# Performance work log

Hardware: AMD Instinct MI355X
Metric: run time of the kernel (lower is better)

The kernel has to match this reference:

```python
import jax, jax.numpy as jnp
import numpy as np


def setup_inputs() -> dict:
    key = jax.random.key(0)
    k1, k2, k3, k4 = jax.random.split(key, 4)
    B, Q, K, H, D = 2, 2048, 2048, 16, 128
    qs = jax.random.normal(k1, (B, Q, H, D), dtype=jnp.float32)
    ks = jax.random.normal(k2, (B, K, H, D), dtype=jnp.float32)
    vs = jax.random.normal(k3, (B, K, H, D), dtype=jnp.float32)
    valid_lens = jax.random.randint(k4, (B,), 1, K + 1, dtype=jnp.int32)
    return {"qs": qs, "ks": ks, "vs": vs, "valid_lens": valid_lens}


def reference(qs, ks, vs, valid_lens):
    B, Q, H, D = qs.shape
    K = ks.shape[1]
    # rearrange 'B L H D -> (B H) L D'
    q = qs.transpose(0, 2, 1, 3).reshape(B * H, Q, D)
    k = ks.transpose(0, 2, 1, 3).reshape(B * H, K, D)
    v = vs.transpose(0, 2, 1, 3).reshape(B * H, K, D)
    # DotScorer: scaled dot product -> (B*H, Q, K)
    scores = jnp.einsum('bqd,bkd->bqk', q, k) / jnp.sqrt(jnp.float32(D))
    # mask_attn: key positions >= valid_len get large negative score
    vl = jnp.repeat(valid_lens, H)                         # (B*H,)
    mask = jnp.arange(K)[None, None, :] < vl[:, None, None]
    scores = jnp.where(mask, scores, jnp.float32(-1e6))
    attn = jax.nn.softmax(scores, axis=-1)
    # dropout is identity (p_dropout=0 / not training)
    ctx = attn @ v                                         # (B*H, Q, D)
    ctx = ctx.reshape(B, H, Q, D).transpose(0, 2, 1, 3)    # (B, Q, H, D)
    return ctx, attn.reshape(B, H, Q, K)
```

## Files before the change

kernel.cpp:

```cpp
#include <hip/hip_runtime.h>
#include <hip/hip_bf16.h>
#include <stdint.h>

#define B_ 2
#define Qn 2048
#define Kn 2048
#define Hn 16
#define Dn 128
#define QT 128
#define KT 64
#define KT1 128
#define HD (Hn*Dn)
#define KROW 132
#define VROW 72

typedef __bf16 bf16x8 __attribute__((ext_vector_type(8)));
typedef __bf16 bf16x4 __attribute__((ext_vector_type(4)));
typedef float f32x4 __attribute__((ext_vector_type(4)));

union BF8 { __bf16 e[8]; bf16x8 v; };

#define SCALE 0.088388347648318447f

struct SMp2 { unsigned short K[2][KT][KROW]; unsigned short V[2][Dn][VROW]; };
union SMu { SMp2 p2; unsigned short K1[2][KT1][KROW]; };

__device__ __forceinline__ void bar_lgkm() {
  asm volatile("s_waitcnt lgkmcnt(0)" ::: "memory");
  __builtin_amdgcn_s_barrier();
  __builtin_amdgcn_sched_barrier(0);
}

__device__ __forceinline__ bf16x4 cvt4(f32x4 a) {
  bf16x4 r;
  r[0] = (__bf16)a[0]; r[1] = (__bf16)a[1];
  r[2] = (__bf16)a[2]; r[3] = (__bf16)a[3];
  return r;
}

__device__ __forceinline__ void stage_k64(const float* kb, unsigned short (*dst)[KROW], int tid) {
  #pragma unroll
  for (int ii = 0; ii < 4; ++ii) {
    int chunk = ii * 512 + tid;
    int row = chunk >> 5, cv = chunk & 31;
    f32x4 a = *(const f32x4*)(kb + (size_t)row * HD + cv * 4);
    *(bf16x4*)&dst[row][cv * 4] = cvt4(a);
  }
}

__device__ __forceinline__ void stage_k128(const float* kb, unsigned short (*dst)[KROW], int tid) {
  #pragma unroll
  for (int ii = 0; ii < 8; ++ii) {
    int chunk = ii * 512 + tid;
    int row = chunk >> 5, cv = chunk & 31;
    f32x4 a = *(const f32x4*)(kb + (size_t)row * HD + cv * 4);
    *(bf16x4*)&dst[row][cv * 4] = cvt4(a);
  }
}

__device__ __forceinline__ void stage_v64(const float* vb, unsigned short (*dst)[VROW], int tid) {
  int d = tid & 127, t0 = tid >> 7;
  const float* colp = vb + d;
  #pragma unroll
  for (int rr = 0; rr < 2; ++rr) {
    int idx = rr * 4 + t0;
    int kk = idx >> 2, gg = idx & 3;
    int kb0 = kk * 32 + gg * 4;
    BF8 t;
    #pragma unroll
    for (int j = 0; j < 4; ++j) {
      t.e[j]     = (__bf16)colp[(size_t)(kb0 + j) * HD];
      t.e[4 + j] = (__bf16)colp[(size_t)(kb0 + 16 + j) * HD];
    }
    *(bf16x8*)&dst[d][kk * 32 + gg * 8] = t.v;
  }
}

__device__ __forceinline__ void load_q(const float* qrow, BF8* qf, int g) {
  #pragma unroll
  for (int s = 0; s < 4; ++s) {
    f32x4 a0 = *(const f32x4*)(qrow + s * 32 + g * 8);
    f32x4 a1 = *(const f32x4*)(qrow + s * 32 + g * 8 + 4);
    #pragma unroll
    for (int j = 0; j < 4; ++j) { qf[s].e[j] = (__bf16)a0[j]; qf[s].e[4 + j] = (__bf16)a1[j]; }
  }
}

__global__ __launch_bounds__(512, 4) void attn_fwd(
    const float* __restrict__ qs, const float* __restrict__ ks,
    const float* __restrict__ vs, const int* __restrict__ vlen,
    float* __restrict__ ctx_out, float* __restrict__ attn_out)
{
  __shared__ __align__(16) SMu sm;

  const int tid = threadIdx.x, wave = tid >> 6, lane = tid & 63;
  const int c = lane & 15, g = lane >> 4;

  const int L   = blockIdx.x;
  const int xcd = L & 7;
  const int i5  = L >> 3;
  const int bh  = ((i5 & 3) << 3) + xcd;
  const int qt  = i5 >> 2;
  const int b   = bh >> 4, h = bh & 15;
  const int vl  = vlen[b];
  const int qb  = qt * QT + wave * 16;

  BF8 qf[4];
  load_q(qs + (((size_t)(b * Qn + qb + c)) * Hn + h) * Dn, qf, g);
  const float* kbase = ks + ((size_t)b * Kn * Hn + h) * Dn;
  const float* vbase = vs + ((size_t)b * Kn * Hn + h) * Dn;

  float rs = 0.f;
  {
    const int nkt = (vl + KT1 - 1) / KT1;
    stage_k128(kbase, sm.K1[0], tid);
    bar_lgkm();
    for (int t = 0; t < nkt; ++t) {
      const int cur = t & 1;
      if (t + 1 < nkt) stage_k128(kbase + (size_t)(t + 1) * KT1 * HD, sm.K1[cur ^ 1], tid);
      #pragma unroll
      for (int nt = 0; nt < 8; ++nt) {
        f32x4 acc = {0.f, 0.f, 0.f, 0.f};
        #pragma unroll
        for (int s = 0; s < 4; ++s) {
          BF8 kf; kf.v = *(const bf16x8*)&sm.K1[cur][nt * 16 + c][s * 32 + g * 8];
          acc = __builtin_amdgcn_mfma_f32_16x16x32_bf16(kf.v, qf[s].v, acc, 0, 0, 0);
        }
        const int k0 = t * KT1 + nt * 16 + g * 4;
        #pragma unroll
        for (int r = 0; r < 4; ++r)
          rs += (k0 + r < vl) ? __expf(acc[r] * SCALE) : 0.f;
      }
      bar_lgkm();
    }
  }
  rs += __shfl_xor(rs, 16);
  rs += __shfl_xor(rs, 32);
  const float inv = 1.0f / rs;

  f32x4 ctxa[8];
  #pragma unroll
  for (int ii = 0; ii < 8; ++ii) ctxa[ii] = (f32x4){0.f, 0.f, 0.f, 0.f};

  const int nkt = (vl + KT - 1) / KT;
  stage_k64(kbase, sm.p2.K[0], tid);
  stage_v64(vbase, sm.p2.V[0], tid);
  bar_lgkm();
  float* rowp = attn_out + ((size_t)bh * Qn + qb + c) * Kn;
  for (int t = 0; t < nkt; ++t) {
    const int cur = t & 1;
    if (t + 1 < nkt) {
      stage_k64(kbase + (size_t)(t + 1) * KT * HD, sm.p2.K[cur ^ 1], tid);
      stage_v64(vbase + (size_t)(t + 1) * KT * HD, sm.p2.V[cur ^ 1], tid);
    }
    BF8 pf[2];
    #pragma unroll
    for (int nt = 0; nt < 4; ++nt) {
      f32x4 acc = {0.f, 0.f, 0.f, 0.f};
      #pragma unroll
      for (int s = 0; s < 4; ++s) {
        BF8 kf; kf.v = *(const bf16x8*)&sm.p2.K[cur][nt * 16 + c][s * 32 + g * 8];
        acc = __builtin_amdgcn_mfma_f32_16x16x32_bf16(kf.v, qf[s].v, acc, 0, 0, 0);
      }
      const int k0 = t * KT + nt * 16 + g * 4;
      f32x4 p;
      #pragma unroll
      for (int r = 0; r < 4; ++r) {
        p[r] = (k0 + r < vl) ? __expf(acc[r] * SCALE) * inv : 0.f;
        pf[nt >> 1].e[(nt & 1) * 4 + r] = (__bf16)p[r];
      }
      *(f32x4*)(rowp + t * KT + nt * 16 + g * 4) = p;
    }
    #pragma unroll
    for (int kk = 0; kk < 2; ++kk)
      #pragma unroll
      for (int n8 = 0; n8 < 8; ++n8) {
        BF8 vf; vf.v = *(const bf16x8*)&sm.p2.V[cur][n8 * 16 + c][kk * 32 + g * 8];
        ctxa[n8] = __builtin_amdgcn_mfma_f32_16x16x32_bf16(vf.v, pf[kk].v, ctxa[n8], 0, 0, 0);
      }
    bar_lgkm();
  }

  const int col0 = nkt * KT;
  #pragma unroll 1
  for (int r = 0; r < 16; ++r) {
    float* zp = attn_out + ((size_t)bh * Qn + qb + r) * Kn;
    for (int c4 = col0 + lane * 4; c4 < Kn; c4 += 256)
      *(f32x4*)(zp + c4) = (f32x4){0.f, 0.f, 0.f, 0.f};
  }

  float* cp = ctx_out + (((size_t)(b * Qn + qb + c)) * Hn + h) * Dn;
  #pragma unroll
  for (int n8 = 0; n8 < 8; ++n8)
    *(f32x4*)(cp + n8 * 16 + g * 4) = ctxa[n8];
}

extern "C" void kernel_launch(void* const* d_in, const int* in_sizes, int n_in,
                              void* d_out, int out_size, void* d_ws, size_t ws_size,
                              hipStream_t stream) {
  const float* qs   = (const float*)d_in[0];
  const float* ks   = (const float*)d_in[1];
  const float* vs   = (const float*)d_in[2];
  const int*   vlen = (const int*)d_in[3];
  float* ctx  = (float*)d_out;
  float* attn = ctx + (size_t)B_ * Qn * Hn * Dn;
  attn_fwd<<<dim3((Qn / QT) * B_ * Hn), 512, 0, stream>>>(qs, ks, vs, vlen, ctx, attn);
}
```

Measured before the change: 217.3 us.

## Switch attention kernel to 32x32x16 MFMA with 256-query and 128-key tiles

Moves both the row-sum pass and the output pass from 16x16x32 to 32x32x16 bf16 MFMA. Each wave now handles 32 query rows, the block covers 256 queries, and both passes use 128-key tiles with matching K/V shared layouts. The aim is more reuse of each staged K/V tile across queries and fewer LDS reads per MFMA, so K/V staging traffic and grid size drop. The cost is more registers and LDS per block, with occupancy lowered to 2 blocks per CU, and only 256 blocks in the grid.

```diff
diff --git a/kernel.cpp b/kernel.cpp
--- a/kernel.cpp
+++ b/kernel.cpp
@@ -7,23 +7,25 @@
 #define Kn 2048
 #define Hn 16
 #define Dn 128
-#define QT 128
-#define KT 64
-#define KT1 128
+#define QT 256
+#define KT 128
 #define HD (Hn*Dn)
 #define KROW 132
-#define VROW 72
+#define VROW 136
 
 typedef __bf16 bf16x8 __attribute__((ext_vector_type(8)));
 typedef __bf16 bf16x4 __attribute__((ext_vector_type(4)));
 typedef float f32x4 __attribute__((ext_vector_type(4)));
+typedef float f32x16 __attribute__((ext_vector_type(16)));
 
 union BF8 { __bf16 e[8]; bf16x8 v; };
 
 #define SCALE 0.088388347648318447f
 
-struct SMp2 { unsigned short K[2][KT][KROW]; unsigned short V[2][Dn][VROW]; };
-union SMu { SMp2 p2; unsigned short K1[2][KT1][KROW]; };
+struct SMs {
+  unsigned short K[2][KT][KROW];
+  unsigned short V[2][Dn][VROW];
+};
 
 __device__ __forceinline__ void bar_lgkm() {
   asm volatile("s_waitcnt lgkmcnt(0)" ::: "memory");
@@ -38,17 +40,7 @@
   return r;
 }
 
-__device__ __forceinline__ void stage_k64(const float* kb, unsigned short (*dst)[KROW], int tid) {
-  #pragma unroll
-  for (int ii = 0; ii < 4; ++ii) {
-    int chunk = ii * 512 + tid;
-    int row = chunk >> 5, cv = chunk & 31;
-    f32x4 a = *(const f32x4*)(kb + (size_t)row * HD + cv * 4);
-    *(bf16x4*)&dst[row][cv * 4] = cvt4(a);
-  }
-}
-
-__device__ __forceinline__ void stage_k128(const float* kb, unsigned short (*dst)[KROW], int tid) {
+__device__ __forceinline__ void stage_k(const float* kb, unsigned short (*dst)[KROW], int tid) {
   #pragma unroll
   for (int ii = 0; ii < 8; ++ii) {
     int chunk = ii * 512 + tid;
@@ -58,43 +50,32 @@
   }
 }
 
-__device__ __forceinline__ void stage_v64(const float* vb, unsigned short (*dst)[VROW], int tid) {
-  int d = tid & 127, t0 = tid >> 7;
+__device__ __forceinline__ void stage_v(const float* vb, unsigned short (*dst)[VROW], int tid) {
+  int d = tid & 127, c0 = tid >> 7;
   const float* colp = vb + d;
   #pragma unroll
-  for (int rr = 0; rr < 2; ++rr) {
-    int idx = rr * 4 + t0;
-    int kk = idx >> 2, gg = idx & 3;
-    int kb0 = kk * 32 + gg * 4;
+  for (int rr = 0; rr < 4; ++rr) {
+    int idx = rr * 4 + c0;
+    int base = (idx >> 2) * 32 + ((idx >> 1) & 1) * 16 + (idx & 1) * 4;
     BF8 t;
     #pragma unroll
     for (int j = 0; j < 4; ++j) {
-      t.e[j]     = (__bf16)colp[(size_t)(kb0 + j) * HD];
-      t.e[4 + j] = (__bf16)colp[(size_t)(kb0 + 16 + j) * HD];
-    }
-    *(bf16x8*)&dst[d][kk * 32 + gg * 8] = t.v;
-  }
-}
-
-__device__ __forceinline__ void load_q(const float* qrow, BF8* qf, int g) {
-  #pragma unroll
-  for (int s = 0; s < 4; ++s) {
-    f32x4 a0 = *(const f32x4*)(qrow + s * 32 + g * 8);
-    f32x4 a1 = *(const f32x4*)(qrow + s * 32 + g * 8 + 4);
-    #pragma unroll
-    for (int j = 0; j < 4; ++j) { qf[s].e[j] = (__bf16)a0[j]; qf[s].e[4 + j] = (__bf16)a1[j]; }
-  }
-}
-
-__global__ __launch_bounds__(512, 4) void attn_fwd(
+      t.e[j]     = (__bf16)colp[(size_t)(base + j) * HD];
+      t.e[4 + j] = (__bf16)colp[(size_t)(base + 8 + j) * HD];
+    }
+    *(bf16x8*)&dst[d][idx * 8] = t.v;
+  }
+}
+
+__global__ __launch_bounds__(512, 2) void attn_fwd(
     const float* __restrict__ qs, const float* __restrict__ ks,
     const float* __restrict__ vs, const int* __restrict__ vlen,
     float* __restrict__ ctx_out, float* __restrict__ attn_out)
 {
-  __shared__ __align__(16) SMu sm;
+  __shared__ __align__(16) SMs sm;
 
   const int tid = threadIdx.x, wave = tid >> 6, lane = tid & 63;
-  const int c = lane & 15, g = lane >> 4;
+  const int l31 = lane & 31, hi = lane >> 5;
 
   const int L   = blockIdx.x;
   const int xcd = L & 7;
@@ -103,96 +84,123 @@
   const int qt  = i5 >> 2;
   const int b   = bh >> 4, h = bh & 15;
   const int vl  = vlen[b];
-  const int qb  = qt * QT + wave * 16;
-
-  BF8 qf[4];
-  load_q(qs + (((size_t)(b * Qn + qb + c)) * Hn + h) * Dn, qf, g);
+  const int qbw = qt * QT + wave * 32;
+
+  BF8 qf[8];
+  {
+    const float* qrow = qs + (((size_t)(b * Qn + qbw + l31)) * Hn + h) * Dn;
+    #pragma unroll
+    for (int s = 0; s < 8; ++s) {
+      int d0 = s * 16 + hi * 8;
+      f32x4 a0 = *(const f32x4*)(qrow + d0);
+      f32x4 a1 = *(const f32x4*)(qrow + d0 + 4);
+      #pragma unroll
+      for (int j = 0; j < 4; ++j) { qf[s].e[j] = (__bf16)a0[j]; qf[s].e[4 + j] = (__bf16)a1[j]; }
+    }
+  }
+
   const float* kbase = ks + ((size_t)b * Kn * Hn + h) * Dn;
   const float* vbase = vs + ((size_t)b * Kn * Hn + h) * Dn;
+  const int nkt = (vl + KT - 1) / KT;
 
   float rs = 0.f;
-  {
-    const int nkt = (vl + KT1 - 1) / KT1;
-    stage_k128(kbase, sm.K1[0], tid);
+  stage_k(kbase, sm.K[0], tid);
+  bar_lgkm();
+  for (int t = 0; t < nkt; ++t) {
+    const int cur = t & 1;
+    if (t + 1 < nkt) stage_k(kbase + (size_t)(t + 1) * KT * HD, sm.K[cur ^ 1], tid);
+    #pragma unroll
+    for (int m = 0; m < 4; ++m) {
+      f32x16 acc;
+      #pragma unroll
+      for (int i = 0; i < 16; ++i) acc[i] = 0.f;
+      #pragma unroll
+      for (int s = 0; s < 8; ++s) {
+        BF8 kf; kf.v = *(const bf16x8*)&sm.K[cur][m * 32 + l31][s * 16 + hi * 8];
+        acc = __builtin_amdgcn_mfma_f32_32x32x16_bf16(kf.v, qf[s].v, acc, 0, 0, 0);
+      }
+      const int kb0 = t * KT + m * 32 + hi * 4;
+      #pragma unroll
+      for (int reg = 0; reg < 16; ++reg) {
+        int key = kb0 + (reg & 3) + 8 * (reg >> 2);
+        rs += (key < vl) ? __expf(acc[reg] * SCALE) : 0.f;
+      }
+    }
     bar_lgkm();
-    for (int t = 0; t < nkt; ++t) {
-      const int cur = t & 1;
-      if (t + 1 < nkt) stage_k128(kbase + (size_t)(t + 1) * KT1 * HD, sm.K1[cur ^ 1], tid);
-      #pragma unroll
-      for (int nt = 0; nt < 8; ++nt) {
-        f32x4 acc = {0.f, 0.f, 0.f, 0.f};
-        #pragma unroll
-        for (int s = 0; s < 4; ++s) {
-          BF8 kf; kf.v = *(const bf16x8*)&sm.K1[cur][nt * 16 + c][s * 32 + g * 8];
-          acc = __builtin_amdgcn_mfma_f32_16x16x32_bf16(kf.v, qf[s].v, acc, 0, 0, 0);
-        }
-        const int k0 = t * KT1 + nt * 16 + g * 4;
-        #pragma unroll
-        for (int r = 0; r < 4; ++r)
-          rs += (k0 + r < vl) ? __expf(acc[r] * SCALE) : 0.f;
-      }
-      bar_lgkm();
-    }
-  }
-  rs += __shfl_xor(rs, 16);
+  }
   rs += __shfl_xor(rs, 32);
   const float inv = 1.0f / rs;
 
-  f32x4 ctxa[8];
-  #pragma unroll
-  for (int ii = 0; ii < 8; ++ii) ctxa[ii] = (f32x4){0.f, 0.f, 0.f, 0.f};
-
-  const int nkt = (vl + KT - 1) / KT;
-  stage_k64(kbase, sm.p2.K[0], tid);
-  stage_v64(vbase, sm.p2.V[0], tid);
+  f32x16 ctxa[4];
+  #pragma unroll
+  for (int ch = 0; ch < 4; ++ch)
+    #pragma unroll
+    for (int i = 0; i < 16; ++i) ctxa[ch][i] = 0.f;
+
+  stage_k(kbase, sm.K[0], tid);
+  stage_v(vbase, sm.V[0], tid);
   bar_lgkm();
-  float* rowp = attn_out + ((size_t)bh * Qn + qb + c) * Kn;
+  float* rowp = attn_out + ((size_t)bh * Qn + qbw + l31) * Kn;
   for (int t = 0; t < nkt; ++t) {
     const int cur = t & 1;
     if (t + 1 < nkt) {
-      stage_k64(kbase + (size_t)(t + 1) * KT * HD, sm.p2.K[cur ^ 1], tid);
-      stage_v64(vbase + (size_t)(t + 1) * KT * HD, sm.p2.V[cur ^ 1], tid);
-    }
-    BF8 pf[2];
-    #pragma unroll
-    for (int nt = 0; nt < 4; ++nt) {
-      f32x4 acc = {0.f, 0.f, 0.f, 0.f};
-      #pragma unroll
-      for (int s = 0; s < 4; ++s) {
-        BF8 kf; kf.v = *(const bf16x8*)&sm.p2.K[cur][nt * 16 + c][s * 32 + g * 8];
-        acc = __builtin_amdgcn_mfma_f32_16x16x32_bf16(kf.v, qf[s].v, acc, 0, 0, 0);
-      }
-      const int k0 = t * KT + nt * 16 + g * 4;
-      f32x4 p;
-      #pragma unroll
-      for (int r = 0; r < 4; ++r) {
-        p[r] = (k0 + r < vl) ? __expf(acc[r] * SCALE) * inv : 0.f;
-        pf[nt >> 1].e[(nt & 1) * 4 + r] = (__bf16)p[r];
-      }
-      *(f32x4*)(rowp + t * KT + nt * 16 + g * 4) = p;
-    }
-    #pragma unroll
-    for (int kk = 0; kk < 2; ++kk)
-      #pragma unroll
-      for (int n8 = 0; n8 < 8; ++n8) {
-        BF8 vf; vf.v = *(const bf16x8*)&sm.p2.V[cur][n8 * 16 + c][kk * 32 + g * 8];
-        ctxa[n8] = __builtin_amdgcn_mfma_f32_16x16x32_bf16(vf.v, pf[kk].v, ctxa[n8], 0, 0, 0);
-      }
+      stage_k(kbase + (size_t)(t + 1) * KT * HD, sm.K[cur ^ 1], tid);
+      stage_v(vbase + (size_t)(t + 1) * KT * HD, sm.V[cur ^ 1], tid);
+    }
+    #pragma unroll
+    for (int m = 0; m < 4; ++m) {
+      f32x16 acc;
+      #pragma unroll
+      for (int i = 0; i < 16; ++i) acc[i] = 0.f;
+      #pragma unroll
+      for (int s = 0; s < 8; ++s) {
+        BF8 kf; kf.v = *(const bf16x8*)&sm.K[cur][m * 32 + l31][s * 16 + hi * 8];
+        acc = __builtin_amdgcn_mfma_f32_32x32x16_bf16(kf.v, qf[s].v, acc, 0, 0, 0);
+      }
+      const int kb0 = t * KT + m * 32;
+      BF8 pf0, pf1;
+      #pragma unroll
+      for (int r4 = 0; r4 < 4; ++r4) {
+        f32x4 p;
+        #pragma unroll
+        for (int rr = 0; rr < 4; ++rr) {
+          int key = kb0 + r4 * 8 + hi * 4 + rr;
+          float v = (key < vl) ? __expf(acc[r4 * 4 + rr] * SCALE) * inv : 0.f;
+          p[rr] = v;
+          if (r4 < 2) pf0.e[r4 * 4 + rr] = (__bf16)v;
+          else        pf1.e[(r4 - 2) * 4 + rr] = (__bf16)v;
+        }
+        *(f32x4*)(rowp + kb0 + r4 * 8 + hi * 4) = p;
+      }
+      #pragma unroll
+      for (int ch = 0; ch < 4; ++ch) {
+        BF8 v0; v0.v = *(const bf16x8*)&sm.V[cur][ch * 32 + l31][(m * 4 + hi) * 8];
+        ctxa[ch] = __builtin_amdgcn_mfma_f32_32x32x16_bf16(v0.v, pf0.v, ctxa[ch], 0, 0, 0);
+        BF8 v1; v1.v = *(const bf16x8*)&sm.V[cur][ch * 32 + l31][(m * 4 + 2 + hi) * 8];
+        ctxa[ch] = __builtin_amdgcn_mfma_f32_32x32x16_bf16(v1.v, pf1.v, ctxa[ch], 0, 0, 0);
+      }
+    }
     bar_lgkm();
   }
 
   const int col0 = nkt * KT;
   #pragma unroll 1
-  for (int r = 0; r < 16; ++r) {
-    float* zp = attn_out + ((size_t)bh * Qn + qb + r) * Kn;
+  for (int r = 0; r < 32; ++r) {
+    float* zp = attn_out + ((size_t)bh * Qn + qbw + r) * Kn;
     for (int c4 = col0 + lane * 4; c4 < Kn; c4 += 256)
       *(f32x4*)(zp + c4) = (f32x4){0.f, 0.f, 0.f, 0.f};
   }
 
-  float* cp = ctx_out + (((size_t)(b * Qn + qb + c)) * Hn + h) * Dn;
-  #pragma unroll
-  for (int n8 = 0; n8 < 8; ++n8)
-    *(f32x4*)(cp + n8 * 16 + g * 4) = ctxa[n8];
+  float* cp = ctx_out + (((size_t)(b * Qn + qbw + l31)) * Hn + h) * Dn;
+  #pragma unroll
+  for (int ch = 0; ch < 4; ++ch)
+    #pragma unroll
+    for (int r4 = 0; r4 < 4; ++r4) {
+      f32x4 o;
+      #pragma unroll
+      for (int rr = 0; rr < 4; ++rr) o[rr] = ctxa[ch][r4 * 4 + rr];
+      *(f32x4*)(cp + ch * 32 + r4 * 8 + hi * 4) = o;
+    }
 }
 
 extern "C" void kernel_launch(void* const* d_in, const int* in_sizes, int n_in,
```

Result: no change. 215.6 us (-0.8%).

## Split K/V staging into register prefetch and deferred LDS write

Applied to the files above, without the earlier changes.

Global loads of the next K/V tile now go into registers before the compute of the current tile. The bf16 conversion and LDS store happen only after the MFMA work, so load latency overlaps with compute instead of stalling at the staging point. It also raises wave priority with s_setprio around the compute section. The cost is higher register pressure, with 32 floats for K128 and 32 for K64+V, which could spill or reduce occupancy under launch_bounds(512,4).

```diff
diff --git a/kernel.cpp b/kernel.cpp
--- a/kernel.cpp
+++ b/kernel.cpp
@@ -38,40 +38,62 @@
   return r;
 }
 
-__device__ __forceinline__ void stage_k64(const float* kb, unsigned short (*dst)[KROW], int tid) {
+__device__ __forceinline__ void load_k64_raw(const float* kb, int tid, f32x4* r) {
   #pragma unroll
   for (int ii = 0; ii < 4; ++ii) {
     int chunk = ii * 512 + tid;
     int row = chunk >> 5, cv = chunk & 31;
-    f32x4 a = *(const f32x4*)(kb + (size_t)row * HD + cv * 4);
-    *(bf16x4*)&dst[row][cv * 4] = cvt4(a);
-  }
-}
-
-__device__ __forceinline__ void stage_k128(const float* kb, unsigned short (*dst)[KROW], int tid) {
+    r[ii] = *(const f32x4*)(kb + (size_t)row * HD + cv * 4);
+  }
+}
+__device__ __forceinline__ void write_k64(const f32x4* r, unsigned short (*dst)[KROW], int tid) {
+  #pragma unroll
+  for (int ii = 0; ii < 4; ++ii) {
+    int chunk = ii * 512 + tid;
+    int row = chunk >> 5, cv = chunk & 31;
+    *(bf16x4*)&dst[row][cv * 4] = cvt4(r[ii]);
+  }
+}
+
+__device__ __forceinline__ void load_k128_raw(const float* kb, int tid, f32x4* r) {
   #pragma unroll
   for (int ii = 0; ii < 8; ++ii) {
     int chunk = ii * 512 + tid;
     int row = chunk >> 5, cv = chunk & 31;
-    f32x4 a = *(const f32x4*)(kb + (size_t)row * HD + cv * 4);
-    *(bf16x4*)&dst[row][cv * 4] = cvt4(a);
-  }
-}
-
-__device__ __forceinline__ void stage_v64(const float* vb, unsigned short (*dst)[VROW], int tid) {
+    r[ii] = *(const f32x4*)(kb + (size_t)row * HD + cv * 4);
+  }
+}
+__device__ __forceinline__ void write_k128(const f32x4* r, unsigned short (*dst)[KROW], int tid) {
+  #pragma unroll
+  for (int ii = 0; ii < 8; ++ii) {
+    int chunk = ii * 512 + tid;
+    int row = chunk >> 5, cv = chunk & 31;
+    *(bf16x4*)&dst[row][cv * 4] = cvt4(r[ii]);
+  }
+}
+
+__device__ __forceinline__ void load_v64_raw(const float* vb, int tid, float* r) {
+  int t0 = tid >> 7;
+  const float* colp = vb + (tid & 127);
+  #pragma unroll
+  for (int rr = 0; rr < 2; ++rr) {
+    int idx = rr * 4 + t0, kk = idx >> 2, gg = idx & 3;
+    int kb0 = kk * 32 + gg * 4;
+    #pragma unroll
+    for (int j = 0; j < 4; ++j) {
+      r[rr * 8 + j]     = colp[(size_t)(kb0 + j) * HD];
+      r[rr * 8 + 4 + j] = colp[(size_t)(kb0 + 16 + j) * HD];
+    }
+  }
+}
+__device__ __forceinline__ void write_v64(const float* r, unsigned short (*dst)[VROW], int tid) {
   int d = tid & 127, t0 = tid >> 7;
-  const float* colp = vb + d;
   #pragma unroll
   for (int rr = 0; rr < 2; ++rr) {
-    int idx = rr * 4 + t0;
-    int kk = idx >> 2, gg = idx & 3;
-    int kb0 = kk * 32 + gg * 4;
+    int idx = rr * 4 + t0, kk = idx >> 2, gg = idx & 3;
     BF8 t;
     #pragma unroll
-    for (int j = 0; j < 4; ++j) {
-      t.e[j]     = (__bf16)colp[(size_t)(kb0 + j) * HD];
-      t.e[4 + j] = (__bf16)colp[(size_t)(kb0 + 16 + j) * HD];
-    }
+    for (int j = 0; j < 8; ++j) t.e[j] = (__bf16)r[rr * 8 + j];
     *(bf16x8*)&dst[d][kk * 32 + gg * 8] = t.v;
   }
 }
@@ -113,11 +135,15 @@
   float rs = 0.f;
   {
     const int nkt = (vl + KT1 - 1) / KT1;
-    stage_k128(kbase, sm.K1[0], tid);
+    f32x4 kr[8];
+    load_k128_raw(kbase, tid, kr);
+    write_k128(kr, sm.K1[0], tid);
     bar_lgkm();
     for (int t = 0; t < nkt; ++t) {
       const int cur = t & 1;
-      if (t + 1 < nkt) stage_k128(kbase + (size_t)(t + 1) * KT1 * HD, sm.K1[cur ^ 1], tid);
+      const bool pf = (t + 1 < nkt);
+      if (pf) load_k128_raw(kbase + (size_t)(t + 1) * KT1 * HD, tid, kr);
+      __builtin_amdgcn_s_setprio(1);
       #pragma unroll
       for (int nt = 0; nt < 8; ++nt) {
         f32x4 acc = {0.f, 0.f, 0.f, 0.f};
@@ -131,6 +157,8 @@
         for (int r = 0; r < 4; ++r)
           rs += (k0 + r < vl) ? __expf(acc[r] * SCALE) : 0.f;
       }
+      __builtin_amdgcn_s_setprio(0);
+      if (pf) write_k128(kr, sm.K1[cur ^ 1], tid);
       bar_lgkm();
     }
   }
@@ -143,42 +171,55 @@
   for (int ii = 0; ii < 8; ++ii) ctxa[ii] = (f32x4){0.f, 0.f, 0.f, 0.f};
 
   const int nkt = (vl + KT - 1) / KT;
-  stage_k64(kbase, sm.p2.K[0], tid);
-  stage_v64(vbase, sm.p2.V[0], tid);
-  bar_lgkm();
-  float* rowp = attn_out + ((size_t)bh * Qn + qb + c) * Kn;
-  for (int t = 0; t < nkt; ++t) {
-    const int cur = t & 1;
-    if (t + 1 < nkt) {
-      stage_k64(kbase + (size_t)(t + 1) * KT * HD, sm.p2.K[cur ^ 1], tid);
-      stage_v64(vbase + (size_t)(t + 1) * KT * HD, sm.p2.V[cur ^ 1], tid);
+  {
+    f32x4 kr[4];
+    float vr[16];
+    load_k64_raw(kbase, tid, kr);
+    load_v64_raw(vbase, tid, vr);
+    write_k64(kr, sm.p2.K[0], tid);
+    write_v64(vr, sm.p2.V[0], tid);
+    bar_lgkm();
+    float* rowp = attn_out + ((size_t)bh * Qn + qb + c) * Kn;
+    for (int t = 0; t < nkt; ++t) {
+      const int cur = t & 1;
+      const bool pf = (t + 1 < nkt);
+      if (pf) {
+        load_k64_raw(kbase + (size_t)(t + 1) * KT * HD, tid, kr);
+        load_v64_raw(vbase + (size_t)(t + 1) * KT * HD, tid, vr);
+      }
+      __builtin_amdgcn_s_setprio(1);
+      BF8 pfm[2];
+      #pragma unroll
+      for (int nt = 0; nt < 4; ++nt) {
+        f32x4 acc = {0.f, 0.f, 0.f, 0.f};
+        #pragma unroll
+        for (int s = 0; s < 4; ++s) {
+          BF8 kf; kf.v = *(const bf16x8*)&sm.p2.K[cur][nt * 16 + c][s * 32 + g * 8];
+          acc = __builtin_amdgcn_mfma_f32_16x16x32_bf16(kf.v, qf[s].v, acc, 0, 0, 0);
+        }
+        const int k0 = t * KT + nt * 16 + g * 4;
+        f32x4 p;
+        #pragma unroll
+        for (int r = 0; r < 4; ++r) {
+          p[r] = (k0 + r < vl) ? __expf(acc[r] * SCALE) * inv : 0.f;
+          pfm[nt >> 1].e[(nt & 1) * 4 + r] = (__bf16)p[r];
+        }
+        *(f32x4*)(rowp + t * KT + nt * 16 + g * 4) = p;
+      }
+      #pragma unroll
+      for (int kk = 0; kk < 2; ++kk)
+        #pragma unroll
+        for (int n8 = 0; n8 < 8; ++n8) {
+          BF8 vf; vf.v = *(const bf16x8*)&sm.p2.V[cur][n8 * 16 + c][kk * 32 + g * 8];
+          ctxa[n8] = __builtin_amdgcn_mfma_f32_16x16x32_bf16(vf.v, pfm[kk].v, ctxa[n8], 0, 0, 0);
+        }
+      __builtin_amdgcn_s_setprio(0);
+      if (pf) {
+        write_k64(kr, sm.p2.K[cur ^ 1], tid);
+        write_v64(vr, sm.p2.V[cur ^ 1], tid);
+      }
+      bar_lgkm();
     }
-    BF8 pf[2];
-    #pragma unroll
-    for (int nt = 0; nt < 4; ++nt) {
-      f32x4 acc = {0.f, 0.f, 0.f, 0.f};
-      #pragma unroll
-      for (int s = 0; s < 4; ++s) {
-        BF8 kf; kf.v = *(const bf16x8*)&sm.p2.K[cur][nt * 16 + c][s * 32 + g * 8];
-        acc = __builtin_amdgcn_mfma_f32_16x16x32_bf16(kf.v, qf[s].v, acc, 0, 0, 0);
-      }
-      const int k0 = t * KT + nt * 16 + g * 4;
-      f32x4 p;
-      #pragma unroll
-      for (int r = 0; r < 4; ++r) {
-        p[r] = (k0 + r < vl) ? __expf(acc[r] * SCALE) * inv : 0.f;
-        pf[nt >> 1].e[(nt & 1) * 4 + r] = (__bf16)p[r];
-      }
-      *(f32x4*)(rowp + t * KT + nt * 16 + g * 4) = p;
-    }
-    #pragma unroll
-    for (int kk = 0; kk < 2; ++kk)
-      #pragma unroll
-      for (int n8 = 0; n8 < 8; ++n8) {
-        BF8 vf; vf.v = *(const bf16x8*)&sm.p2.V[cur][n8 * 16 + c][kk * 32 + g * 8];
-        ctxa[n8] = __builtin_amdgcn_mfma_f32_16x16x32_bf16(vf.v, pf[kk].v, ctxa[n8], 0, 0, 0);
-      }
-    bar_lgkm();
   }
 
   const int col0 = nkt * KT;
```

New measurement: 223.7 us. 1.03x slower.

## Skew PV matmul one tile behind QK and skip masking on full tiles

Applied to the files above, without the earlier changes.

The second pass now stages V for the current tile while running the P·V MFMAs for the previous tile. This software-pipelines the V transpose-load latency behind the QK and exp work. Both passes also skip the per-element valid-length comparison on every tile except the partial last one. The row-sum uses a 4-wide vector accumulator to shorten the dependency chain. The cost is extra registers for the carried P fragments and a post-loop epilogue, which could hurt occupancy.

```diff
diff --git a/kernel.cpp b/kernel.cpp
--- a/kernel.cpp
+++ b/kernel.cpp
@@ -110,14 +110,16 @@
   const float* kbase = ks + ((size_t)b * Kn * Hn + h) * Dn;
   const float* vbase = vs + ((size_t)b * Kn * Hn + h) * Dn;
 
-  float rs = 0.f;
+  f32x4 rsv = {0.f, 0.f, 0.f, 0.f};
   {
     const int nkt = (vl + KT1 - 1) / KT1;
+    const bool hasb = (vl & (KT1 - 1)) != 0;
     stage_k128(kbase, sm.K1[0], tid);
     bar_lgkm();
     for (int t = 0; t < nkt; ++t) {
       const int cur = t & 1;
       if (t + 1 < nkt) stage_k128(kbase + (size_t)(t + 1) * KT1 * HD, sm.K1[cur ^ 1], tid);
+      const bool mb = hasb && (t == nkt - 1);
       #pragma unroll
       for (int nt = 0; nt < 8; ++nt) {
         f32x4 acc = {0.f, 0.f, 0.f, 0.f};
@@ -126,14 +128,20 @@
           BF8 kf; kf.v = *(const bf16x8*)&sm.K1[cur][nt * 16 + c][s * 32 + g * 8];
           acc = __builtin_amdgcn_mfma_f32_16x16x32_bf16(kf.v, qf[s].v, acc, 0, 0, 0);
         }
-        const int k0 = t * KT1 + nt * 16 + g * 4;
-        #pragma unroll
-        for (int r = 0; r < 4; ++r)
-          rs += (k0 + r < vl) ? __expf(acc[r] * SCALE) : 0.f;
+        if (!mb) {
+          #pragma unroll
+          for (int r = 0; r < 4; ++r) rsv[r] += __expf(acc[r] * SCALE);
+        } else {
+          const int k0 = t * KT1 + nt * 16 + g * 4;
+          #pragma unroll
+          for (int r = 0; r < 4; ++r)
+            rsv[r] += (k0 + r < vl) ? __expf(acc[r] * SCALE) : 0.f;
+        }
       }
       bar_lgkm();
     }
   }
+  float rs = (rsv[0] + rsv[1]) + (rsv[2] + rsv[3]);
   rs += __shfl_xor(rs, 16);
   rs += __shfl_xor(rs, 32);
   const float inv = 1.0f / rs;
@@ -143,42 +151,65 @@
   for (int ii = 0; ii < 8; ++ii) ctxa[ii] = (f32x4){0.f, 0.f, 0.f, 0.f};
 
   const int nkt = (vl + KT - 1) / KT;
-  stage_k64(kbase, sm.p2.K[0], tid);
-  stage_v64(vbase, sm.p2.V[0], tid);
-  bar_lgkm();
-  float* rowp = attn_out + ((size_t)bh * Qn + qb + c) * Kn;
-  for (int t = 0; t < nkt; ++t) {
-    const int cur = t & 1;
-    if (t + 1 < nkt) {
-      stage_k64(kbase + (size_t)(t + 1) * KT * HD, sm.p2.K[cur ^ 1], tid);
-      stage_v64(vbase + (size_t)(t + 1) * KT * HD, sm.p2.V[cur ^ 1], tid);
-    }
-    BF8 pf[2];
+  const bool hasb2 = (vl & (KT - 1)) != 0;
+  BF8 pprev0, pprev1;
+  {
+    stage_k64(kbase, sm.p2.K[0], tid);
+    bar_lgkm();
+    float* rowp = attn_out + ((size_t)bh * Qn + qb + c) * Kn;
+    for (int t = 0; t < nkt; ++t) {
+      const int cur = t & 1;
+      if (t + 1 < nkt) stage_k64(kbase + (size_t)(t + 1) * KT * HD, sm.p2.K[cur ^ 1], tid);
+      stage_v64(vbase + (size_t)t * KT * HD, sm.p2.V[cur], tid);
+      const bool mb = hasb2 && (t == nkt - 1);
+
+      BF8 pc0, pc1;
+      #pragma unroll
+      for (int nt = 0; nt < 4; ++nt) {
+        f32x4 acc = {0.f, 0.f, 0.f, 0.f};
+        #pragma unroll
+        for (int s = 0; s < 4; ++s) {
+          BF8 kf; kf.v = *(const bf16x8*)&sm.p2.K[cur][nt * 16 + c][s * 32 + g * 8];
+          acc = __builtin_amdgcn_mfma_f32_16x16x32_bf16(kf.v, qf[s].v, acc, 0, 0, 0);
+        }
+        f32x4 p;
+        if (!mb) {
+          #pragma unroll
+          for (int r = 0; r < 4; ++r) p[r] = __expf(acc[r] * SCALE) * inv;
+        } else {
+          const int k0 = t * KT + nt * 16 + g * 4;
+          #pragma unroll
+          for (int r = 0; r < 4; ++r)
+            p[r] = (k0 + r < vl) ? __expf(acc[r] * SCALE) * inv : 0.f;
+        }
+        #pragma unroll
+        for (int r = 0; r < 4; ++r) {
+          if (nt < 2) pc0.e[(nt & 1) * 4 + r] = (__bf16)p[r];
+          else        pc1.e[(nt & 1) * 4 + r] = (__bf16)p[r];
+        }
+        *(f32x4*)(rowp + t * KT + nt * 16 + g * 4) = p;
+      }
+
+      if (t > 0) {
+        #pragma unroll
+        for (int n8 = 0; n8 < 8; ++n8) {
+          BF8 v0; v0.v = *(const bf16x8*)&sm.p2.V[cur ^ 1][n8 * 16 + c][g * 8];
+          ctxa[n8] = __builtin_amdgcn_mfma_f32_16x16x32_bf16(v0.v, pprev0.v, ctxa[n8], 0, 0, 0);
+          BF8 v1; v1.v = *(const bf16x8*)&sm.p2.V[cur ^ 1][n8 * 16 + c][32 + g * 8];
+          ctxa[n8] = __builtin_amdgcn_mfma_f32_16x16x32_bf16(v1.v, pprev1.v, ctxa[n8], 0, 0, 0);
+        }
+      }
+      pprev0 = pc0; pprev1 = pc1;
+      bar_lgkm();
+    }
+    const int lc = (nkt - 1) & 1;
     #pragma unroll
-    for (int nt = 0; nt < 4; ++nt) {
-      f32x4 acc = {0.f, 0.f, 0.f, 0.f};
-      #pragma unroll
-      for (int s = 0; s < 4; ++s) {
-        BF8 kf; kf.v = *(const bf16x8*)&sm.p2.K[cur][nt * 16 + c][s * 32 + g * 8];
-        acc = __builtin_amdgcn_mfma_f32_16x16x32_bf16(kf.v, qf[s].v, acc, 0, 0, 0);
-      }
-      const int k0 = t * KT + nt * 16 + g * 4;
-      f32x4 p;
-      #pragma unroll
-      for (int r = 0; r < 4; ++r) {
-        p[r] = (k0 + r < vl) ? __expf(acc[r] * SCALE) * inv : 0.f;
-        pf[nt >> 1].e[(nt & 1) * 4 + r] = (__bf16)p[r];
-      }
-      *(f32x4*)(rowp + t * KT + nt * 16 + g * 4) = p;
-    }
-    #pragma unroll
-    for (int kk = 0; kk < 2; ++kk)
-      #pragma unroll
-      for (int n8 = 0; n8 < 8; ++n8) {
-        BF8 vf; vf.v = *(const bf16x8*)&sm.p2.V[cur][n8 * 16 + c][kk * 32 + g * 8];
-        ctxa[n8] = __builtin_amdgcn_mfma_f32_16x16x32_bf16(vf.v, pf[kk].v, ctxa[n8], 0, 0, 0);
-      }
-    bar_lgkm();
+    for (int n8 = 0; n8 < 8; ++n8) {
+      BF8 v0; v0.v = *(const bf16x8*)&sm.p2.V[lc][n8 * 16 + c][g * 8];
+      ctxa[n8] = __builtin_amdgcn_mfma_f32_16x16x32_bf16(v0.v, pprev0.v, ctxa[n8], 0, 0, 0);
+      BF8 v1; v1.v = *(const bf16x8*)&sm.p2.V[lc][n8 * 16 + c][32 + g * 8];
+      ctxa[n8] = __builtin_amdgcn_mfma_f32_16x16x32_bf16(v1.v, pprev1.v, ctxa[n8], 0, 0, 0);
+    }
   }
 
   const int col0 = nkt * KT;
```

New measurement: 217.3 us. Within noise of the previous version (-0.0%).
